# Optimization experiments

Hardware: AMD Instinct MI355X
Metric: run time of the kernel (lower is better)

## Reference

```python
import jax, jax.numpy as jnp
import numpy as np

D_MODEL = 1024
N_HEADS = 16
D_HEAD = 64  # = d_model // num_heads = d_inner
LN_EPS = 1e-5


def setup_inputs() -> dict:
    key = jax.random.key(0)
    ks = jax.random.split(key, 8)
    B, CUR, PREV = 2, 1024, 1024
    T = CUR + PREV
    s = 0.02
    return {
        "x": jax.random.normal(ks[0], (B, CUR, D_MODEL), jnp.float32),
        "pos_emb": jax.random.normal(ks[1], (T, D_MODEL), jnp.float32),
        "u": jax.random.normal(ks[2], (N_HEADS, D_HEAD), jnp.float32),
        "v": jax.random.normal(ks[3], (N_HEADS, D_HEAD), jnp.float32),
        "tgt_mask": jnp.ones((B, CUR, T, 1), jnp.bool_),
        "mem": jax.random.normal(ks[4], (B, PREV, D_MODEL), jnp.float32),
        "Wq": jax.random.normal(ks[5], (D_MODEL, D_MODEL), jnp.float32) * s,
        "Wkv": jax.random.normal(ks[6], (2 * D_MODEL, D_MODEL), jnp.float32) * s,
        "Wfc": jax.random.normal(ks[7], (D_MODEL, D_MODEL), jnp.float32) * s,
        "bfc": jnp.zeros((D_MODEL,), jnp.float32),
        "gamma": jnp.ones((D_MODEL,), jnp.float32),
        "beta": jnp.zeros((D_MODEL,), jnp.float32),
    }


def _rel_shift(x):
    # Faithful port of the torch _rel_shift: pad along the query axis (dim=1),
    # reinterpret the contiguous buffer as (I+1, B, J, H), drop first row, reshape back.
    B, I, J, H = x.shape
    zero_pad = jnp.zeros((B, 1, J, H), x.dtype)
    x_padded = jnp.concatenate([zero_pad, x], axis=1).reshape(I + 1, B, J, H)
    return x_padded[1:].reshape(B, I, J, H)


def reference(x, pos_emb, u, v, tgt_mask, mem, Wq, Wkv, Wfc, bfc, gamma, beta):
    B, CUR, _ = x.shape
    h = jnp.concatenate([mem, x], axis=1)          # (B, T, d_model)
    T = h.shape[1]
    q = (x @ Wq.T).reshape(B, CUR, N_HEADS, D_HEAD)
    kv = h @ Wkv.T                                  # (B, T, 2*d_model)
    k, vv = jnp.split(kv, 2, axis=-1)
    k = k.reshape(B, T, N_HEADS, D_HEAD)
    vv = vv.reshape(B, T, N_HEADS, D_HEAD)

    content_attn = jnp.einsum('bihd,bjhd->bijh', q + u, k)
    pe = pos_emb.reshape(T, N_HEADS, D_HEAD)
    pos_attn = _rel_shift(jnp.einsum('bihd,jhd->bijh', q + v, pe))

    attn = content_attn + pos_attn                  # (B, I, J, H)
    attn = jnp.where(tgt_mask == 0, -jnp.inf, attn)  # mask BEFORE scaling (as original)
    attn = attn / (D_HEAD ** 0.5)
    attn = jax.nn.softmax(attn, axis=1)             # NOTE: original softmaxes over dim=1 (query axis)

    weighted = jnp.einsum('bijh,bjhd->bihd', attn, vv).reshape(B, CUR, -1)
    y = x + weighted @ Wfc.T + bfc                  # residual + fc (post-norm path)
    mu = jnp.mean(y, axis=-1, keepdims=True)
    var = jnp.var(y, axis=-1, keepdims=True)
    return (y - mu) / jnp.sqrt(var + LN_EPS) * gamma + beta
```

## Files before the change

kernel.cpp:

```cpp
#include <hip/hip_runtime.h>

#define DM   1024
#define CUR  1024
#define TT   2048

typedef float  f32x4  __attribute__((ext_vector_type(4)));
typedef __bf16 bf16_t;
typedef __bf16 bf16x8 __attribute__((ext_vector_type(8)));
typedef __bf16 bf16x4 __attribute__((ext_vector_type(4)));
typedef short  s16x4  __attribute__((ext_vector_type(4)));

#define SCALE_A 0.18033688f

static __device__ __forceinline__ float exp2fast(float x) { return __builtin_amdgcn_exp2f(x); }
static __device__ __forceinline__ float log2fast(float x) { return __builtin_amdgcn_logf(x); }

static __device__ __forceinline__ f32x4 mfma32(bf16x8 a, bf16x8 b, f32x4 c) {
  return __builtin_amdgcn_mfma_f32_16x16x32_bf16(a, b, c, 0, 0, 0);
}
static __device__ __forceinline__ f32x4 mfma16(bf16x4 a, bf16x4 b, f32x4 c) {
  return __builtin_amdgcn_mfma_f32_16x16x16bf16_1k(
      __builtin_bit_cast(s16x4, a), __builtin_bit_cast(s16x4, b), c, 0, 0, 0);
}
static __device__ __forceinline__ void gl_lds16(const bf16_t* g, bf16_t* l) {
  __builtin_amdgcn_global_load_lds(
      (const __attribute__((address_space(1))) void*)g,
      (__attribute__((address_space(3))) void*)l, 16, 0, 0);
}


__global__ __launch_bounds__(256) void wconv_kernel(const float* __restrict__ Wq,
                                                    const float* __restrict__ Wkv,
                                                    const float* __restrict__ Wfc,
                                                    bf16_t* __restrict__ wqb,
                                                    bf16_t* __restrict__ wkvb,
                                                    bf16_t* __restrict__ wfcb) {
  int t = blockIdx.x * 256 + threadIdx.x;
  const float* src; bf16_t* dst; int off;
  if (t < 262144)      { src = Wq;  dst = wqb;  off = t; }
  else if (t < 786432) { src = Wkv; dst = wkvb; off = t - 262144; }
  else                 { src = Wfc; dst = wfcb; off = t - 786432; }
  f32x4 v = *(const f32x4*)(src + (size_t)off * 4);
  bf16x4 o;
  o[0] = (bf16_t)v[0]; o[1] = (bf16_t)v[1]; o[2] = (bf16_t)v[2]; o[3] = (bf16_t)v[3];
  *(bf16x4*)(dst + (size_t)off * 4) = o;
}

__global__ __launch_bounds__(256) void conv_h_kernel(const float* __restrict__ mem,
                                                     const float* __restrict__ x,
                                                     bf16_t* __restrict__ hb) {
  int t = blockIdx.x * 256 + threadIdx.x;
  int idx = t << 2;
  int b   = idx >> 21;
  int rem = idx & ((1 << 21) - 1);
  int tt  = rem >> 10;
  int c   = rem & 1023;
  const float* s = (tt < 1024)
      ? (mem + ((size_t)b * 1024 + tt) * DM + c)
      : (x   + ((size_t)b * 1024 + (tt - 1024)) * DM + c);
  f32x4 v = *(const f32x4*)s;
  bf16x4 o;
  o[0] = (bf16_t)v[0]; o[1] = (bf16_t)v[1]; o[2] = (bf16_t)v[2]; o[3] = (bf16_t)v[3];
  *(bf16x4*)(hb + idx) = o;
}

__global__ __launch_bounds__(256) void pe_fill_kernel(const float* __restrict__ pos_emb,
                                                      bf16_t* __restrict__ Bs) {
  int t  = blockIdx.x * 256 + threadIdx.x;
  int d4 = (t & 15) << 2;
  int j  = (t >> 4) & 2047;
  int bh = t >> 15;
  int h  = bh & 15;
  f32x4 v = *(const f32x4*)(pos_emb + (size_t)j * DM + h * 64 + d4);
  bf16x4 o;
  o[0] = (bf16_t)v[0]; o[1] = (bf16_t)v[1]; o[2] = (bf16_t)v[2]; o[3] = (bf16_t)v[3];
  *(bf16x4*)(Bs + ((size_t)bh * TT + j) * 128 + 64 + d4) = o;
}

template<int WM>
__device__ __forceinline__ void gemm_core(const bf16_t* __restrict__ A,
                                          const bf16_t* __restrict__ B,
                                          int r0, int c0,
                                          bf16_t* At, bf16_t* Bt,
                                          f32x4 (&acc)[WM][4]) {
  const int ASZ = WM * 1024;
  const int BSZ = 4096;
  const int tid = threadIdx.x, w = tid >> 6, l = tid & 63;
  const int lm = l & 15, q = l >> 4;
  const int wrow = w >> 1, wcol = w & 1;
  const int gg  = (l & 3) ^ ((l >> 3) & 3);
  const int rsw = (lm >> 1) & 3;
  const bf16_t* gA = A + (size_t)(r0 + w * (WM / 2) * 16 + (l >> 2)) * 1024 + gg * 8;
  const bf16_t* gB = B + (size_t)(c0 + w * 32 + (l >> 2)) * 1024 + gg * 8;
  bf16_t* lA = At + w * (WM / 2) * 512;
  bf16_t* lB = Bt + w * 1024;
  const bf16_t* fA = At + (wrow * WM * 16 + lm) * 32;
  const bf16_t* fB = Bt + (wcol * 64 + lm) * 32;
#pragma unroll
  for (int t2 = 0; t2 < WM / 2; ++t2) gl_lds16(gA + (size_t)t2 * 16384, lA + t2 * 512);
#pragma unroll
  for (int t2 = 0; t2 < 2; ++t2)      gl_lds16(gB + (size_t)t2 * 16384, lB + t2 * 512);
  __syncthreads();
  int p = 0;
  for (int k0 = 0; k0 < 1024; k0 += 32) {
    int pn = p ^ 1;
    if (k0 < 992) {
#pragma unroll
      for (int t2 = 0; t2 < WM / 2; ++t2)
        gl_lds16(gA + (size_t)t2 * 16384 + k0 + 32, lA + pn * ASZ + t2 * 512);
#pragma unroll
      for (int t2 = 0; t2 < 2; ++t2)
        gl_lds16(gB + (size_t)t2 * 16384 + k0 + 32, lB + pn * BSZ + t2 * 512);
    }
    bf16x8 af[WM], bfm[4];
#pragma unroll
    for (int it = 0; it < WM; ++it)
      af[it] = *(const bf16x8*)(fA + p * ASZ + it * 512 + ((q ^ rsw) << 3));
#pragma unroll
    for (int jt = 0; jt < 4; ++jt)
      bfm[jt] = *(const bf16x8*)(fB + p * BSZ + jt * 512 + ((q ^ rsw) << 3));
#pragma unroll
    for (int it = 0; it < WM; ++it)
#pragma unroll
      for (int jt = 0; jt < 4; ++jt)
        acc[it][jt] = mfma32(af[it], bfm[jt], acc[it][jt]);
    __syncthreads();
    p = pn;
  }
}

__global__ __launch_bounds__(256) void k1_q(const bf16_t* __restrict__ hb,
                                            const bf16_t* __restrict__ Wqb,
                                            const float* __restrict__ u,
                                            const float* __restrict__ v,
                                            bf16_t* __restrict__ As) {
  __shared__ union { struct { bf16_t At[4096]; bf16_t Bt[8192]; } m; float Tt[4][272]; } sm;
  int blk = blockIdx.x;
  int r0 = (blk >> 3) * 64, c0 = (blk & 7) * 128;
  int b = r0 >> 10;
  const bf16_t* Axv = hb + ((size_t)(b + 1) << 20);
  f32x4 acc[2][4] = {};
  gemm_core<2>(Axv, Wqb, r0, c0, sm.m.At, sm.m.Bt, acc);
  const int tid = threadIdx.x, w = tid >> 6, l = tid & 63;
  const int lm = l & 15, q = l >> 4;
  const int wrow = w >> 1, wcol = w & 1;
  float* Tw = sm.Tt[w];
  int h = (c0 + wcol * 64) >> 6;
#pragma unroll
  for (int it = 0; it < 2; ++it) {
#pragma unroll
    for (int jt = 0; jt < 4; ++jt) {
#pragma unroll
      for (int r = 0; r < 4; ++r) Tw[(q * 4 + r) * 17 + lm] = acc[it][jt][r];
      __builtin_amdgcn_wave_barrier();
      int row = r0 + wrow * 32 + it * 16 + lm;
      int ii = row & 1023;
      int cbase = c0 + wcol * 64 + jt * 16 + q * 4;
      int d0 = cbase & 63;
      f32x4 u4 = *(const f32x4*)(u + cbase);
      f32x4 v4 = *(const f32x4*)(v + cbase);
      f32x4 tv;
#pragma unroll
      for (int e = 0; e < 4; ++e) tv[e] = Tw[lm * 17 + q * 4 + e];
      bf16x4 oc, op;
#pragma unroll
      for (int e = 0; e < 4; ++e) {
        oc[e] = (bf16_t)((tv[e] + u4[e]) * SCALE_A);
        op[e] = (bf16_t)((tv[e] + v4[e]) * SCALE_A);
      }
      *(bf16x4*)(As + (((size_t)(b * 16 + h)) * CUR + ii) * 128 + d0) = oc;
      if (b == 0) {
        if (ii >= 1)
          *(bf16x4*)(As + (((size_t)h) * CUR + (ii - 1)) * 128 + 64 + d0) = op;
        if (ii == 1023) {
          bf16x4 z = {};
          *(bf16x4*)(As + (((size_t)h) * CUR + 1023) * 128 + 64 + d0) = z;
        }
      } else {
        *(bf16x4*)(As + (((size_t)(16 + h)) * CUR + ii) * 128 + 64 + d0) = op;
      }
      __builtin_amdgcn_wave_barrier();
    }
  }
}

__global__ __launch_bounds__(256) void k2_kv(const bf16_t* __restrict__ hb,
                                             const bf16_t* __restrict__ Wkvb,
                                             bf16_t* __restrict__ Bs,
                                             bf16_t* __restrict__ vvT) {
  __shared__ union { struct { bf16_t At[8192]; bf16_t Bt[8192]; } m; float Tt[4][272]; } sm;
  int blk = blockIdx.x;
  int xcd = blk & 7, t = blk >> 3;
  int r0 = (t & 31) * 128;
  int c0 = (xcd * 2 + (t >> 5)) * 128;
  f32x4 acc[4][4] = {};
  gemm_core<4>(hb, Wkvb, r0, c0, sm.m.At, sm.m.Bt, acc);
  const int tid = threadIdx.x, w = tid >> 6, l = tid & 63;
  const int lm = l & 15, q = l >> 4;
  const int wrow = w >> 1, wcol = w & 1;
  int b = r0 >> 11;
  if (c0 < 1024) {
    float* Tw = sm.Tt[w];
    int h = (c0 + wcol * 64) >> 6;
#pragma unroll
    for (int it = 0; it < 4; ++it) {
#pragma unroll
      for (int jt = 0; jt < 4; ++jt) {
#pragma unroll
        for (int r = 0; r < 4; ++r) Tw[(q * 4 + r) * 17 + lm] = acc[it][jt][r];
        __builtin_amdgcn_wave_barrier();
        int j = (r0 + wrow * 64 + it * 16 + lm) & 2047;
        int d0 = jt * 16 + q * 4;
        bf16x4 o;
#pragma unroll
        for (int e = 0; e < 4; ++e) o[e] = (bf16_t)Tw[lm * 17 + q * 4 + e];
        *(bf16x4*)(Bs + (((size_t)(b * 16 + h)) * TT + j) * 128 + d0) = o;
        __builtin_amdgcn_wave_barrier();
      }
    }
  } else {
#pragma unroll
    for (int it = 0; it < 4; ++it) {
#pragma unroll
      for (int jt = 0; jt < 4; ++jt) {
        int c2 = c0 + wcol * 64 + jt * 16 + lm - 1024;
        int h = c2 >> 6, d = c2 & 63;
        int j = (r0 + wrow * 64 + it * 16 + q * 4) & 2047;
        bf16x4 o;
#pragma unroll
        for (int r = 0; r < 4; ++r) o[r] = (bf16_t)acc[it][jt][r];
        *(bf16x4*)(vvT + (((size_t)(b * 16 + h)) * 64 + d) * TT + j) = o;
      }
    }
  }
}

__global__ __launch_bounds__(256) void k3_stats(const bf16_t* __restrict__ As,
                                                const bf16_t* __restrict__ Bs,
                                                float* __restrict__ LL) {
  __shared__ bf16_t At[2 * 8192];
  const int tid = threadIdx.x, w = tid >> 6, l = tid & 63;
  const int lm = l & 15, q = l >> 4;
  const int gg  = (l & 3) ^ ((l >> 3) & 3);
  const int rsw = (lm >> 1) & 3;
  int blk = blockIdx.x;
  int xcd = blk & 7, t = blk >> 3;
  int jblk = t & 15, bh = xcd * 4 + (t >> 4);
  int j0 = jblk * 128;
  const bf16_t* bsrow = Bs + ((size_t)bh * TT + j0 + w * 32 + lm) * 128 + q * 8;
  bf16x8 bfr[2][4];
#pragma unroll
  for (int js = 0; js < 2; ++js)
#pragma unroll
    for (int kt = 0; kt < 4; ++kt)
      bfr[js][kt] = *(const bf16x8*)(bsrow + js * 2048 + kt * 32);
  const bf16_t* abase = As + (size_t)bh * CUR * 128 + (size_t)(l >> 2) * 128 + w * 32 + gg * 8;
  bf16_t* lA = At + w * 2048;
  const bf16_t* fA = At + lm * 32;
  float m0 = -3.0e38f, l0 = 0.f, m1 = -3.0e38f, l1 = 0.f;
#pragma unroll
  for (int t2 = 0; t2 < 4; ++t2)
    gl_lds16(abase + (size_t)t2 * 16 * 128, lA + t2 * 512);
  __syncthreads();
  int p = 0;
  for (int ib = 0; ib < 16; ++ib) {
    int pn = p ^ 1;
    if (ib < 15) {
#pragma unroll
      for (int t2 = 0; t2 < 4; ++t2)
        gl_lds16(abase + (size_t)((ib + 1) * 64 + t2 * 16) * 128, lA + pn * 8192 + t2 * 512);
    }
#pragma unroll
    for (int isub = 0; isub < 4; ++isub) {
      bf16x8 af[4];
#pragma unroll
      for (int kt = 0; kt < 4; ++kt)
        af[kt] = *(const bf16x8*)(fA + p * 8192 + kt * 2048 + isub * 512 + ((q ^ rsw) << 3));
      f32x4 s0 = {}, s1 = {};
#pragma unroll
      for (int kt = 0; kt < 4; ++kt) {
        s0 = mfma32(af[kt], bfr[0][kt], s0);
        s1 = mfma32(af[kt], bfr[1][kt], s1);
      }
      float tm = fmaxf(fmaxf(s0[0], s0[1]), fmaxf(s0[2], s0[3]));
      float nm = fmaxf(m0, tm);
      l0 = l0 * exp2fast(m0 - nm) + exp2fast(s0[0] - nm) + exp2fast(s0[1] - nm) +
           exp2fast(s0[2] - nm) + exp2fast(s0[3] - nm);
      m0 = nm;
      tm = fmaxf(fmaxf(s1[0], s1[1]), fmaxf(s1[2], s1[3]));
      nm = fmaxf(m1, tm);
      l1 = l1 * exp2fast(m1 - nm) + exp2fast(s1[0] - nm) + exp2fast(s1[1] - nm) +
           exp2fast(s1[2] - nm) + exp2fast(s1[3] - nm);
      m1 = nm;
    }
    __syncthreads();
    p = pn;
  }
#pragma unroll
  for (int off = 16; off <= 32; off <<= 1) {
    float m2 = __shfl_xor(m0, off, 64), l2 = __shfl_xor(l0, off, 64);
    float nm = fmaxf(m0, m2);
    l0 = l0 * exp2fast(m0 - nm) + l2 * exp2fast(m2 - nm);
    m0 = nm;
    m2 = __shfl_xor(m1, off, 64); l2 = __shfl_xor(l1, off, 64);
    nm = fmaxf(m1, m2);
    l1 = l1 * exp2fast(m1 - nm) + l2 * exp2fast(m2 - nm);
    m1 = nm;
  }
  if (l < 16) {
    LL[(size_t)bh * TT + j0 + w * 32 + l]      = m0 + log2fast(l0);
    LL[(size_t)bh * TT + j0 + w * 32 + 16 + l] = m1 + log2fast(l1);
  }
}

__global__ __launch_bounds__(256) void k4_attnv(const bf16_t* __restrict__ As,
                                                const bf16_t* __restrict__ Bs,
                                                const bf16_t* __restrict__ vvT,
                                                const float* __restrict__ LL,
                                                float* __restrict__ Pp) {
  __shared__ union {
    struct { bf16_t Bt[2 * 8192]; bf16_t Vt[2 * 4096]; } m;
    float Tt[4][1088];
  } sm;
  int blk = blockIdx.x;
  int xcd = blk & 7, tb = blk >> 3;
  int iblk = tb & 7, pl = tb >> 3;
  int bh = xcd * 4 + (pl >> 1), jch = pl & 1;
  int b = bh >> 4, h = bh & 15;
  int i0 = iblk * 128;
  int jbase = jch * 1024;
  const int tid = threadIdx.x, w = tid >> 6, l = tid & 63;
  const int lm = l & 15, q = l >> 4;
  const int gg  = (l & 3) ^ ((l >> 3) & 3);
  const int rsw = (lm >> 1) & 3;
  const bf16_t* ar = As + (size_t)bh * CUR * 128 + (size_t)(i0 + w * 32 + lm) * 128 + q * 8;
  bf16x8 bi[2][4];
#pragma unroll
  for (int is = 0; is < 2; ++is)
#pragma unroll
    for (int kt = 0; kt < 4; ++kt)
      bi[is][kt] = *(const bf16x8*)(ar + is * 2048 + kt * 32);
  const bf16_t* bbase = Bs + ((size_t)bh * TT + jbase) * 128 + (size_t)(l >> 2) * 128 + w * 32 + gg * 8;
  int inst0 = w * 2, inst1 = w * 2 + 1;
  const bf16_t* vsrc0 = vvT + ((size_t)bh * 64 + (inst0 & 3) * 16 + (l >> 2)) * TT + jbase +
                        (inst0 >> 2) * 32 + gg * 8;
  const bf16_t* vsrc1 = vvT + ((size_t)bh * 64 + (inst1 & 3) * 16 + (l >> 2)) * TT + jbase +
                        (inst1 >> 2) * 32 + gg * 8;
  bf16_t* vdst0 = sm.m.Vt + (inst0 >> 2) * 2048 + (inst0 & 3) * 512;
  bf16_t* vdst1 = sm.m.Vt + (inst1 >> 2) * 2048 + (inst1 & 3) * 512;
  bf16_t* lB = sm.m.Bt + w * 2048;
  const float* llb = LL + (size_t)bh * TT + jbase;
  f32x4 acc0[4] = {}, acc1[4] = {};
#pragma unroll
  for (int t2 = 0; t2 < 4; ++t2)
    gl_lds16(bbase + (size_t)t2 * 16 * 128, lB + t2 * 512);
  gl_lds16(vsrc0, vdst0);
  gl_lds16(vsrc1, vdst1);
  __syncthreads();
  int p = 0;
  for (int jb = 0; jb < 16; ++jb) {
    int pn = p ^ 1;
    if (jb < 15) {
      const bf16_t* bs2 = bbase + (size_t)(jb + 1) * 64 * 128;
#pragma unroll
      for (int t2 = 0; t2 < 4; ++t2)
        gl_lds16(bs2 + (size_t)t2 * 16 * 128, lB + pn * 8192 + t2 * 512);
      gl_lds16(vsrc0 + (jb + 1) * 64, vdst0 + pn * 4096);
      gl_lds16(vsrc1 + (jb + 1) * 64, vdst1 + pn * 4096);
    }
    const bf16_t* fB = sm.m.Bt + p * 8192 + lm * 32;
    const bf16_t* vf = sm.m.Vt + p * 4096 + lm * 32;
#pragma unroll
    for (int js = 0; js < 4; ++js) {
      bf16x8 af[4];
#pragma unroll
      for (int kt = 0; kt < 4; ++kt)
        af[kt] = *(const bf16x8*)(fB + kt * 2048 + js * 512 + ((q ^ rsw) << 3));
      f32x4 s0 = {}, s1 = {};
#pragma unroll
      for (int kt = 0; kt < 4; ++kt) {
        s0 = mfma32(af[kt], bi[0][kt], s0);
        s1 = mfma32(af[kt], bi[1][kt], s1);
      }
      f32x4 ll = *(const f32x4*)(llb + jb * 64 + js * 16 + q * 4);
      bf16x4 p0, p1;
#pragma unroll
      for (int e = 0; e < 4; ++e) {
        p0[e] = (bf16_t)exp2fast(s0[e] - ll[e]);
        p1[e] = (bf16_t)exp2fast(s1[e] - ll[e]);
      }
      int vg = ((js & 1) << 1) | (q >> 1);
      const bf16_t* vfa = vf + (js >> 1) * 2048 + ((vg ^ rsw) << 3) + ((q & 1) << 2);
#pragma unroll
      for (int dt = 0; dt < 4; ++dt) {
        bf16x4 a2 = *(const bf16x4*)(vfa + dt * 512);
        acc0[dt] = mfma16(a2, p0, acc0[dt]);
        acc1[dt] = mfma16(a2, p1, acc1[dt]);
      }
    }
    __syncthreads();
    p = pn;
  }
  float* Tw = sm.Tt[w];
  float* pout = Pp + ((size_t)jch << 21);
  int ir = l >> 2, dc = (l & 3) * 16;
#pragma unroll
  for (int is = 0; is < 2; ++is) {
#pragma unroll
    for (int dt = 0; dt < 4; ++dt) {
      f32x4 a = is ? acc1[dt] : acc0[dt];
#pragma unroll
      for (int r = 0; r < 4; ++r) Tw[(dt * 16 + q * 4 + r) * 17 + lm] = a[r];
    }
    __builtin_amdgcn_wave_barrier();
    int i = i0 + w * 32 + is * 16 + ir;
    float* orow = pout + ((size_t)(b * CUR + i)) * DM + h * 64 + dc;
#pragma unroll
    for (int e4 = 0; e4 < 4; ++e4) {
      f32x4 o;
#pragma unroll
      for (int e = 0; e < 4; ++e) o[e] = Tw[(dc + e4 * 4 + e) * 17 + ir];
      *(f32x4*)(orow + e4 * 4) = o;
    }
    __builtin_amdgcn_wave_barrier();
  }
}

__global__ __launch_bounds__(256) void k4_reduce(const float* __restrict__ P,
                                                 bf16_t* __restrict__ wbuf) {
  int t = blockIdx.x * 256 + threadIdx.x;
  f32x4 a = *(const f32x4*)(P + (size_t)t * 4);
  f32x4 c = *(const f32x4*)(P + (1u << 21) + (size_t)t * 4);
  bf16x4 o;
#pragma unroll
  for (int e = 0; e < 4; ++e) o[e] = (bf16_t)(a[e] + c[e]);
  *(bf16x4*)(wbuf + (size_t)t * 4) = o;
}

__global__ __launch_bounds__(256) void k5_fc(const bf16_t* __restrict__ wb,
                                             const bf16_t* __restrict__ Wfcb,
                                             const float* __restrict__ x,
                                             const float* __restrict__ bfc,
                                             float* __restrict__ y) {
  __shared__ union { struct { bf16_t At[4096]; bf16_t Bt[8192]; } m; float Tt[4][272]; } sm;
  int blk = blockIdx.x;
  int r0 = (blk >> 3) * 64, c0 = (blk & 7) * 128;
  f32x4 acc[2][4] = {};
  gemm_core<2>(wb, Wfcb, r0, c0, sm.m.At, sm.m.Bt, acc);
  const int tid = threadIdx.x, w = tid >> 6, l = tid & 63;
  const int lm = l & 15, q = l >> 4;
  const int wrow = w >> 1, wcol = w & 1;
  float* Tw = sm.Tt[w];
#pragma unroll
  for (int it = 0; it < 2; ++it) {
#pragma unroll
    for (int jt = 0; jt < 4; ++jt) {
#pragma unroll
      for (int r = 0; r < 4; ++r) Tw[(q * 4 + r) * 17 + lm] = acc[it][jt][r];
      __builtin_amdgcn_wave_barrier();
      int row = r0 + wrow * 32 + it * 16 + lm;
      int cb = c0 + wcol * 64 + jt * 16 + q * 4;
      f32x4 xb4 = *(const f32x4*)(x + (size_t)row * DM + cb);
      f32x4 bf4 = *(const f32x4*)(bfc + cb);
      f32x4 o;
#pragma unroll
      for (int e = 0; e < 4; ++e) o[e] = Tw[lm * 17 + q * 4 + e] + xb4[e] + bf4[e];
      *(f32x4*)(y + (size_t)row * DM + cb) = o;
      __builtin_amdgcn_wave_barrier();
    }
  }
}

__global__ __launch_bounds__(256) void k6_ln(const float* __restrict__ y,
                                             const float* __restrict__ gamma,
                                             const float* __restrict__ beta,
                                             float* __restrict__ out) {
  int row = blockIdx.x, t = threadIdx.x;
  const float* yr = y + (size_t)row * DM;
  f32x4 v = *(const f32x4*)(yr + t * 4);
  float s = v[0] + v[1] + v[2] + v[3];
  float ss = v[0] * v[0] + v[1] * v[1] + v[2] * v[2] + v[3] * v[3];
#pragma unroll
  for (int off = 1; off < 64; off <<= 1) {
    s += __shfl_xor(s, off, 64);
    ss += __shfl_xor(ss, off, 64);
  }
  __shared__ float ps[4], pss[4];
  int wv = t >> 6, ln = t & 63;
  if (ln == 0) { ps[wv] = s; pss[wv] = ss; }
  __syncthreads();
  s = ps[0] + ps[1] + ps[2] + ps[3];
  ss = pss[0] + pss[1] + pss[2] + pss[3];
  float mu = s * (1.0f / DM);
  float var = ss * (1.0f / DM) - mu * mu;
  float rstd = rsqrtf(var + 1e-5f);
  f32x4 g = *(const f32x4*)(gamma + t * 4);
  f32x4 bb = *(const f32x4*)(beta + t * 4);
  f32x4 o;
#pragma unroll
  for (int e = 0; e < 4; ++e) o[e] = (v[e] - mu) * rstd * g[e] + bb[e];
  *(f32x4*)(out + (size_t)row * DM + t * 4) = o;
}

extern "C" void kernel_launch(void* const* d_in, const int* in_sizes, int n_in,
                              void* d_out, int out_size, void* d_ws, size_t ws_size,
                              hipStream_t stream) {
  const float* x    = (const float*)d_in[0];
  const float* pos  = (const float*)d_in[1];
  const float* u    = (const float*)d_in[2];
  const float* v    = (const float*)d_in[3];
  const float* mem  = (const float*)d_in[5];
  const float* Wq   = (const float*)d_in[6];
  const float* Wkv  = (const float*)d_in[7];
  const float* Wfc  = (const float*)d_in[8];
  const float* bfc  = (const float*)d_in[9];
  const float* gam  = (const float*)d_in[10];
  const float* bet  = (const float*)d_in[11];
  float* out = (float*)d_out;

  char* ws = (char*)d_ws;
  const size_t MB = 1ull << 20;
  bf16_t* hb   = (bf16_t*)(ws);
  bf16_t* wqb  = (bf16_t*)(ws + 8 * MB);
  bf16_t* wkvb = (bf16_t*)(ws + 10 * MB);
  bf16_t* wfcb = (bf16_t*)(ws + 14 * MB);
  bf16_t* As   = (bf16_t*)(ws + 16 * MB);
  bf16_t* Bs   = (bf16_t*)(ws + 24 * MB);
  bf16_t* vvT  = (bf16_t*)(ws + 40 * MB);
  float*  LL   = (float*) (ws + 48 * MB);
  bf16_t* wbuf = (bf16_t*)(ws + 49 * MB);
  float*  y    = (float*) (ws + 53 * MB);
  float*  Pp   = (float*) (ws + 61 * MB);

  wconv_kernel<<<4096, 256, 0, stream>>>(Wq, Wkv, Wfc, wqb, wkvb, wfcb);
  conv_h_kernel<<<4096, 256, 0, stream>>>(mem, x, hb);
  pe_fill_kernel<<<4096, 256, 0, stream>>>(pos, Bs);

  k1_q<<<256, 256, 0, stream>>>(hb, wqb, u, v, As);
  k2_kv<<<512, 256, 0, stream>>>(hb, wkvb, Bs, vvT);

  k3_stats<<<512, 256, 0, stream>>>(As, Bs, LL);
  k4_attnv<<<512, 256, 0, stream>>>(As, Bs, vvT, LL, Pp);
  k4_reduce<<<2048, 256, 0, stream>>>(Pp, wbuf);

  k5_fc<<<256, 256, 0, stream>>>(wbuf, wfcb, x, bfc, y);
  k6_ln<<<2048, 256, 0, stream>>>(y, gam, bet, out);
}
```

Before: 251.0 us.

## Split attention stats and attn-V over more blocks, fuse prep conversions

```diff
diff --git a/kernel.cpp b/kernel.cpp
--- a/kernel.cpp
+++ b/kernel.cpp
@@ -28,53 +28,52 @@
       (__attribute__((address_space(3))) void*)l, 16, 0, 0);
 }
 
-
-__global__ __launch_bounds__(256) void wconv_kernel(const float* __restrict__ Wq,
-                                                    const float* __restrict__ Wkv,
-                                                    const float* __restrict__ Wfc,
-                                                    bf16_t* __restrict__ wqb,
-                                                    bf16_t* __restrict__ wkvb,
-                                                    bf16_t* __restrict__ wfcb) {
+__global__ __launch_bounds__(256) void prep_kernel(const float* __restrict__ Wq,
+                                                   const float* __restrict__ Wkv,
+                                                   const float* __restrict__ Wfc,
+                                                   const float* __restrict__ mem,
+                                                   const float* __restrict__ x,
+                                                   const float* __restrict__ pos,
+                                                   bf16_t* __restrict__ wqb,
+                                                   bf16_t* __restrict__ wkvb,
+                                                   bf16_t* __restrict__ wfcb,
+                                                   bf16_t* __restrict__ hb,
+                                                   bf16_t* __restrict__ Bs) {
   int t = blockIdx.x * 256 + threadIdx.x;
-  const float* src; bf16_t* dst; int off;
-  if (t < 262144)      { src = Wq;  dst = wqb;  off = t; }
-  else if (t < 786432) { src = Wkv; dst = wkvb; off = t - 262144; }
-  else                 { src = Wfc; dst = wfcb; off = t - 786432; }
-  f32x4 v = *(const f32x4*)(src + (size_t)off * 4);
-  bf16x4 o;
-  o[0] = (bf16_t)v[0]; o[1] = (bf16_t)v[1]; o[2] = (bf16_t)v[2]; o[3] = (bf16_t)v[3];
-  *(bf16x4*)(dst + (size_t)off * 4) = o;
-}
-
-__global__ __launch_bounds__(256) void conv_h_kernel(const float* __restrict__ mem,
-                                                     const float* __restrict__ x,
-                                                     bf16_t* __restrict__ hb) {
-  int t = blockIdx.x * 256 + threadIdx.x;
-  int idx = t << 2;
-  int b   = idx >> 21;
-  int rem = idx & ((1 << 21) - 1);
-  int tt  = rem >> 10;
-  int c   = rem & 1023;
-  const float* s = (tt < 1024)
-      ? (mem + ((size_t)b * 1024 + tt) * DM + c)
-      : (x   + ((size_t)b * 1024 + (tt - 1024)) * DM + c);
-  f32x4 v = *(const f32x4*)s;
-  bf16x4 o;
-  o[0] = (bf16_t)v[0]; o[1] = (bf16_t)v[1]; o[2] = (bf16_t)v[2]; o[3] = (bf16_t)v[3];
-  *(bf16x4*)(hb + idx) = o;
-}
-
-__global__ __launch_bounds__(256) void pe_fill_kernel(const float* __restrict__ pos_emb,
-                                                      bf16_t* __restrict__ Bs) {
-  int t  = blockIdx.x * 256 + threadIdx.x;
-  int d4 = (t & 15) << 2;
-  int j  = (t >> 4) & 2047;
-  int bh = t >> 15;
-  int h  = bh & 15;
-  f32x4 v = *(const f32x4*)(pos_emb + (size_t)j * DM + h * 64 + d4);
-  bf16x4 o;
-  o[0] = (bf16_t)v[0]; o[1] = (bf16_t)v[1]; o[2] = (bf16_t)v[2]; o[3] = (bf16_t)v[3];
-  *(bf16x4*)(Bs + ((size_t)bh * TT + j) * 128 + 64 + d4) = o;
+  if (t < (1 << 20)) {
+    const float* src; bf16_t* dst; int off;
+    if (t < 262144)      { src = Wq;  dst = wqb;  off = t; }
+    else if (t < 786432) { src = Wkv; dst = wkvb; off = t - 262144; }
+    else                 { src = Wfc; dst = wfcb; off = t - 786432; }
+    f32x4 v = *(const f32x4*)(src + (size_t)off * 4);
+    bf16x4 o;
+    o[0] = (bf16_t)v[0]; o[1] = (bf16_t)v[1]; o[2] = (bf16_t)v[2]; o[3] = (bf16_t)v[3];
+    *(bf16x4*)(dst + (size_t)off * 4) = o;
+  } else if (t < (2 << 20)) {
+    int th = t - (1 << 20);
+    int idx = th << 2;
+    int b   = idx >> 21;
+    int rem = idx & ((1 << 21) - 1);
+    int tt  = rem >> 10;
+    int c   = rem & 1023;
+    const float* s = (tt < 1024)
+        ? (mem + ((size_t)b * 1024 + tt) * DM + c)
+        : (x   + ((size_t)b * 1024 + (tt - 1024)) * DM + c);
+    f32x4 v = *(const f32x4*)s;
+    bf16x4 o;
+    o[0] = (bf16_t)v[0]; o[1] = (bf16_t)v[1]; o[2] = (bf16_t)v[2]; o[3] = (bf16_t)v[3];
+    *(bf16x4*)(hb + idx) = o;
+  } else {
+    int tp = t - (2 << 20);
+    int d4 = (tp & 15) << 2;
+    int j  = (tp >> 4) & 2047;
+    int bh = tp >> 15;
+    int h  = bh & 15;
+    f32x4 v = *(const f32x4*)(pos + (size_t)j * DM + h * 64 + d4);
+    bf16x4 o;
+    o[0] = (bf16_t)v[0]; o[1] = (bf16_t)v[1]; o[2] = (bf16_t)v[2]; o[3] = (bf16_t)v[3];
+    *(bf16x4*)(Bs + ((size_t)bh * TT + j) * 128 + 64 + d4) = o;
+  }
 }
 
 template<int WM>
@@ -237,7 +236,7 @@
 
 __global__ __launch_bounds__(256) void k3_stats(const bf16_t* __restrict__ As,
                                                 const bf16_t* __restrict__ Bs,
-                                                float* __restrict__ LL) {
+                                                float* __restrict__ Lp) {
   __shared__ bf16_t At[2 * 8192];
   const int tid = threadIdx.x, w = tid >> 6, l = tid & 63;
   const int lm = l & 15, q = l >> 4;
@@ -245,7 +244,7 @@
   const int rsw = (lm >> 1) & 3;
   int blk = blockIdx.x;
   int xcd = blk & 7, t = blk >> 3;
-  int jblk = t & 15, bh = xcd * 4 + (t >> 4);
+  int jblk = t & 15, ich = (t >> 4) & 1, bh = xcd * 4 + (t >> 5);
   int j0 = jblk * 128;
   const bf16_t* bsrow = Bs + ((size_t)bh * TT + j0 + w * 32 + lm) * 128 + q * 8;
   bf16x8 bfr[2][4];
@@ -254,18 +253,19 @@
 #pragma unroll
     for (int kt = 0; kt < 4; ++kt)
       bfr[js][kt] = *(const bf16x8*)(bsrow + js * 2048 + kt * 32);
-  const bf16_t* abase = As + (size_t)bh * CUR * 128 + (size_t)(l >> 2) * 128 + w * 32 + gg * 8;
+  const bf16_t* abase = As + (size_t)bh * CUR * 128 +
+                        (size_t)(ich * 512 + (l >> 2)) * 128 + w * 32 + gg * 8;
   bf16_t* lA = At + w * 2048;
   const bf16_t* fA = At + lm * 32;
-  float m0 = -3.0e38f, l0 = 0.f, m1 = -3.0e38f, l1 = 0.f;
+  float l0 = 0.f, l1 = 0.f;
 #pragma unroll
   for (int t2 = 0; t2 < 4; ++t2)
     gl_lds16(abase + (size_t)t2 * 16 * 128, lA + t2 * 512);
   __syncthreads();
   int p = 0;
-  for (int ib = 0; ib < 16; ++ib) {
+  for (int ib = 0; ib < 8; ++ib) {
     int pn = p ^ 1;
-    if (ib < 15) {
+    if (ib < 7) {
 #pragma unroll
       for (int t2 = 0; t2 < 4; ++t2)
         gl_lds16(abase + (size_t)((ib + 1) * 64 + t2 * 16) * 128, lA + pn * 8192 + t2 * 512);
@@ -282,35 +282,33 @@
         s0 = mfma32(af[kt], bfr[0][kt], s0);
         s1 = mfma32(af[kt], bfr[1][kt], s1);
       }
-      float tm = fmaxf(fmaxf(s0[0], s0[1]), fmaxf(s0[2], s0[3]));
-      float nm = fmaxf(m0, tm);
-      l0 = l0 * exp2fast(m0 - nm) + exp2fast(s0[0] - nm) + exp2fast(s0[1] - nm) +
-           exp2fast(s0[2] - nm) + exp2fast(s0[3] - nm);
-      m0 = nm;
-      tm = fmaxf(fmaxf(s1[0], s1[1]), fmaxf(s1[2], s1[3]));
-      nm = fmaxf(m1, tm);
-      l1 = l1 * exp2fast(m1 - nm) + exp2fast(s1[0] - nm) + exp2fast(s1[1] - nm) +
-           exp2fast(s1[2] - nm) + exp2fast(s1[3] - nm);
-      m1 = nm;
+      l0 += exp2fast(s0[0]) + exp2fast(s0[1]) + exp2fast(s0[2]) + exp2fast(s0[3]);
+      l1 += exp2fast(s1[0]) + exp2fast(s1[1]) + exp2fast(s1[2]) + exp2fast(s1[3]);
     }
     __syncthreads();
     p = pn;
   }
 #pragma unroll
   for (int off = 16; off <= 32; off <<= 1) {
-    float m2 = __shfl_xor(m0, off, 64), l2 = __shfl_xor(l0, off, 64);
-    float nm = fmaxf(m0, m2);
-    l0 = l0 * exp2fast(m0 - nm) + l2 * exp2fast(m2 - nm);
-    m0 = nm;
-    m2 = __shfl_xor(m1, off, 64); l2 = __shfl_xor(l1, off, 64);
-    nm = fmaxf(m1, m2);
-    l1 = l1 * exp2fast(m1 - nm) + l2 * exp2fast(m2 - nm);
-    m1 = nm;
+    l0 += __shfl_xor(l0, off, 64);
+    l1 += __shfl_xor(l1, off, 64);
   }
   if (l < 16) {
-    LL[(size_t)bh * TT + j0 + w * 32 + l]      = m0 + log2fast(l0);
-    LL[(size_t)bh * TT + j0 + w * 32 + 16 + l] = m1 + log2fast(l1);
-  }
+    float* lp = Lp + (size_t)ich * 65536 + (size_t)bh * TT + j0 + w * 32;
+    lp[l]      = l0;
+    lp[16 + l] = l1;
+  }
+}
+
+__global__ __launch_bounds__(256) void k3_comb(const float* __restrict__ Lp,
+                                               float* __restrict__ LL) {
+  int t = blockIdx.x * 256 + threadIdx.x;
+  f32x4 a = *(const f32x4*)(Lp + (size_t)t * 4);
+  f32x4 b = *(const f32x4*)(Lp + 65536 + (size_t)t * 4);
+  f32x4 o;
+#pragma unroll
+  for (int e = 0; e < 4; ++e) o[e] = log2fast(a[e] + b[e]);
+  *(f32x4*)(LL + (size_t)t * 4) = o;
 }
 
 __global__ __launch_bounds__(256) void k4_attnv(const bf16_t* __restrict__ As,
@@ -325,10 +323,10 @@
   int blk = blockIdx.x;
   int xcd = blk & 7, tb = blk >> 3;
   int iblk = tb & 7, pl = tb >> 3;
-  int bh = xcd * 4 + (pl >> 1), jch = pl & 1;
+  int bh = xcd * 4 + (pl >> 2), jch = pl & 3;
   int b = bh >> 4, h = bh & 15;
   int i0 = iblk * 128;
-  int jbase = jch * 1024;
+  int jbase = jch * 512;
   const int tid = threadIdx.x, w = tid >> 6, l = tid & 63;
   const int lm = l & 15, q = l >> 4;
   const int gg  = (l & 3) ^ ((l >> 3) & 3);
@@ -358,9 +356,9 @@
   gl_lds16(vsrc1, vdst1);
   __syncthreads();
   int p = 0;
-  for (int jb = 0; jb < 16; ++jb) {
+  for (int jb = 0; jb < 8; ++jb) {
     int pn = p ^ 1;
-    if (jb < 15) {
+    if (jb < 7) {
       const bf16_t* bs2 = bbase + (size_t)(jb + 1) * 64 * 128;
 #pragma unroll
       for (int t2 = 0; t2 < 4; ++t2)
@@ -430,10 +428,12 @@
                                                  bf16_t* __restrict__ wbuf) {
   int t = blockIdx.x * 256 + threadIdx.x;
   f32x4 a = *(const f32x4*)(P + (size_t)t * 4);
-  f32x4 c = *(const f32x4*)(P + (1u << 21) + (size_t)t * 4);
+  f32x4 b = *(const f32x4*)(P + (1u << 21) + (size_t)t * 4);
+  f32x4 c = *(const f32x4*)(P + (2u << 21) + (size_t)t * 4);
+  f32x4 d = *(const f32x4*)(P + (3u << 21) + (size_t)t * 4);
   bf16x4 o;
 #pragma unroll
-  for (int e = 0; e < 4; ++e) o[e] = (bf16_t)(a[e] + c[e]);
+  for (int e = 0; e < 4; ++e) o[e] = (bf16_t)((a[e] + b[e]) + (c[e] + d[e]));
   *(bf16x4*)(wbuf + (size_t)t * 4) = o;
 }
 
@@ -523,24 +523,24 @@
   bf16_t* hb   = (bf16_t*)(ws);
   bf16_t* wqb  = (bf16_t*)(ws + 8 * MB);
   bf16_t* wkvb = (bf16_t*)(ws + 10 * MB);
-  bf16_t* wfcb = (bf16_t*)(ws + 14 * MB);
-  bf16_t* As   = (bf16_t*)(ws + 16 * MB);
-  bf16_t* Bs   = (bf16_t*)(ws + 24 * MB);
-  bf16_t* vvT  = (bf16_t*)(ws + 40 * MB);
+  bf16_t* As   = (bf16_t*)(ws + 14 * MB);
+  bf16_t* Bs   = (bf16_t*)(ws + 22 * MB);
+  bf16_t* vvT  = (bf16_t*)(ws + 38 * MB);
+  bf16_t* wfcb = (bf16_t*)(ws + 46 * MB);
   float*  LL   = (float*) (ws + 48 * MB);
-  bf16_t* wbuf = (bf16_t*)(ws + 49 * MB);
-  float*  y    = (float*) (ws + 53 * MB);
-  float*  Pp   = (float*) (ws + 61 * MB);
-
-  wconv_kernel<<<4096, 256, 0, stream>>>(Wq, Wkv, Wfc, wqb, wkvb, wfcb);
-  conv_h_kernel<<<4096, 256, 0, stream>>>(mem, x, hb);
-  pe_fill_kernel<<<4096, 256, 0, stream>>>(pos, Bs);
-
+  float*  Lp   = (float*) (ws + 48 * MB + 262144);
+  float*  Pp   = (float*) (ws + 49 * MB);
+  bf16_t* wbuf = (bf16_t*)(ws);
+  float*  y    = (float*) (ws + 4 * MB);
+
+  prep_kernel<<<12288, 256, 0, stream>>>(Wq, Wkv, Wfc, mem, x, pos,
+                                         wqb, wkvb, wfcb, hb, Bs);
   k1_q<<<256, 256, 0, stream>>>(hb, wqb, u, v, As);
   k2_kv<<<512, 256, 0, stream>>>(hb, wkvb, Bs, vvT);
 
-  k3_stats<<<512, 256, 0, stream>>>(As, Bs, LL);
-  k4_attnv<<<512, 256, 0, stream>>>(As, Bs, vvT, LL, Pp);
+  k3_stats<<<1024, 256, 0, stream>>>(As, Bs, Lp);
+  k3_comb<<<64, 256, 0, stream>>>(Lp, LL);
+  k4_attnv<<<1024, 256, 0, stream>>>(As, Bs, vvT, LL, Pp);
   k4_reduce<<<2048, 256, 0, stream>>>(Pp, wbuf);
 
   k5_fc<<<256, 256, 0, stream>>>(wbuf, wfcb, x, bfc, y);
```

New measurement: 246.6 us. Within noise of the previous version (-1.8%).
